# Performance work log

Measured on AMD Instinct MI355X. Metric: run time of the kernel, lower is better.

The kernel has to match this reference:

```python
import jax, jax.numpy as jnp
import numpy as np
import math

D_MODEL = 256
NUM_SLOTS = 128
RANK = 32
STEPS = 6
VOCAB = 32000
SEQ = 512
BATCH = 8
LN_EPS = 1e-5


def setup_inputs() -> dict:
    key = jax.random.key(0)
    ks = jax.random.split(key, 16)
    std = 0.02
    inp = {
        "input_ids": jax.random.randint(ks[0], (BATCH, SEQ), 0, VOCAB),
        "attention_mask": jnp.ones((BATCH, SEQ), dtype=jnp.int32),
        "token_emb": jax.random.normal(ks[1], (VOCAB, D_MODEL), jnp.float32) * std,
        "pos_emb": jax.random.normal(ks[2], (SEQ, D_MODEL), jnp.float32) * std,
        "H": jax.random.normal(ks[3], (NUM_SLOTS, D_MODEL), jnp.float32) / math.sqrt(D_MODEL),
        "W_source": jax.random.normal(ks[4], (NUM_SLOTS, NUM_SLOTS, D_MODEL, RANK), jnp.float32) * std,
        "W_target": jax.random.normal(ks[5], (NUM_SLOTS, NUM_SLOTS, RANK, D_MODEL), jnp.float32) * std,
        "Wq_in": jax.random.normal(ks[6], (D_MODEL, D_MODEL), jnp.float32) / math.sqrt(D_MODEL),
        "Wk_slots": jax.random.normal(ks[7], (D_MODEL, D_MODEL), jnp.float32) / math.sqrt(D_MODEL),
        "Wv_in": jax.random.normal(ks[8], (D_MODEL, D_MODEL), jnp.float32) / math.sqrt(D_MODEL),
        "Wq_out": jax.random.normal(ks[9], (D_MODEL, D_MODEL), jnp.float32) / math.sqrt(D_MODEL),
        "Wk_fin": jax.random.normal(ks[10], (D_MODEL, D_MODEL), jnp.float32) / math.sqrt(D_MODEL),
        "Wv_fin": jax.random.normal(ks[11], (D_MODEL, D_MODEL), jnp.float32) / math.sqrt(D_MODEL),
        "W_out_proj": jax.random.normal(ks[12], (VOCAB, D_MODEL), jnp.float32) / math.sqrt(D_MODEL),
        "ln_scale": jnp.ones((STEPS, D_MODEL), jnp.float32),
        "ln_bias": jnp.zeros((STEPS, D_MODEL), jnp.float32),
    }
    return inp


def _layernorm(x, g, b):
    mu = jnp.mean(x, axis=-1, keepdims=True)
    var = jnp.var(x, axis=-1, keepdims=True)
    return (x - mu) / jnp.sqrt(var + LN_EPS) * g + b


def _forward(input_ids, attention_mask, token_emb, pos_emb, H, W_source, W_target,
             Wq_in, Wk_slots, Wv_in, Wq_out, Wk_fin, Wv_fin, W_out_proj, ln_scale, ln_bias):
    B, L = input_ids.shape
    scale = 1.0 / math.sqrt(D_MODEL)
    # embeddings (dropout is identity in eval)
    X = token_emb[input_ids] + pos_emb[jnp.arange(L)][None]  # (B,L,D)
    # compress: input tokens -> slots
    Q_in = X @ Wq_in.T                      # (B,L,D)
    K_sl = H @ Wk_slots.T                   # (S,D)
    V_in = X @ Wv_in.T                      # (B,L,D)
    A = jax.nn.softmax(Q_in @ K_sl.T * scale, axis=-1)  # (B,L,S)
    m = attention_mask.astype(A.dtype)[..., None]
    A = A * m
    A = A / (jnp.sum(A, axis=1, keepdims=True) + 1e-8)
    IR = jnp.einsum('bls,bld->bsd', A, V_in)            # (B,S,D)
    H_state = H[None] + IR                               # (B,S,D)

    off_diag = (1.0 - jnp.eye(NUM_SLOTS, dtype=H_state.dtype))  # (S,S)

    def step(h, lnp):
        g, b = lnp
        # bilinear slot-to-slot influence; contract directly, no (B,S,S,D) expand of h
        inter = jnp.einsum('bid,ijdr->bijr', h, W_source)        # (B,S,S,R)
        out = jnp.einsum('bijr,ijrd->bijd', inter, W_target)     # (B,S,S,D)
        infl = jnp.einsum('bijd,ij->bjd', out, off_diag)         # mask diag + sum over i
        h = _layernorm(h + jax.nn.relu(infl), g, b)
        return h, None

    H_state, _ = jax.lax.scan(step, H_state, (ln_scale, ln_bias))

    # expand: slots -> tokens
    Q_out = X @ Wq_out.T                   # (B,L,D)
    K_f = H_state @ Wk_fin.T               # (B,S,D)
    V_f = H_state @ Wv_fin.T               # (B,S,D)
    A2 = jax.nn.softmax(jnp.einsum('bld,bsd->bls', Q_out, K_f) * scale, axis=-1)
    Y = jnp.einsum('bls,bsd->bld', A2, V_f)
    logits = Y @ W_out_proj.T              # (B,L,V)
    return logits


def reference(input_ids, attention_mask, token_emb, pos_emb, H, W_source, W_target,
              Wq_in, Wk_slots, Wv_in, Wq_out, Wk_fin, Wv_fin, W_out_proj, ln_scale, ln_bias):
    return _forward(input_ids, attention_mask, token_emb, pos_emb, H, W_source, W_target,
                    Wq_in, Wk_slots, Wv_in, Wq_out, Wk_fin, Wv_fin, W_out_proj, ln_scale, ln_bias)
```

## Files before the change

kernel.cpp:

```cpp
#include <hip/hip_runtime.h>
#include <hip/hip_bf16.h>
#include <math.h>

#define D_MODEL 256
#define NUM_SLOTS 128
#define RANK 32
#define N_STEPS 6
#define VOCAB 32000
#define SEQ 512
#define BATCH 8
#define NTOK (BATCH*SEQ)
#define LN_EPS 1e-5f
#define SM_SCALE 0.0625f
#define IGROUPS 8
#define IPG (NUM_SLOTS/IGROUPS)

typedef __attribute__((ext_vector_type(8))) short bf16x8;
typedef __attribute__((ext_vector_type(8))) _Float16 f16x8;
typedef __attribute__((ext_vector_type(4))) float f32x4;

#define GLD_LDS16(g, l) __builtin_amdgcn_global_load_lds( \
    (const __attribute__((address_space(1))) unsigned int*)(g), \
    (__attribute__((address_space(3))) unsigned int*)(l), 16, 0, 0)

__device__ inline unsigned short f2bf(float x) {
    unsigned u = __float_as_uint(x);
    unsigned r = u + 0x7fff + ((u >> 16) & 1);
    return (unsigned short)(r >> 16);
}
__device__ inline float bf2f(unsigned short h) {
    return __uint_as_float(((unsigned)h) << 16);
}
__device__ inline unsigned pk2(float a, float b) {
    auto v = __builtin_amdgcn_cvt_pkrtz(a, b);
    union { decltype(v) x; unsigned u; } c;
    c.x = v;
    return c.u;
}
__device__ inline unsigned short f2h(float x) {
    union { _Float16 h; unsigned short u; } c;
    c.h = (_Float16)x;
    return c.u;
}
__device__ inline float h2f(unsigned short u) {
    union { unsigned short u; _Float16 h; } c;
    c.u = u;
    return (float)c.h;
}

__global__ __launch_bounds__(256) void k_embed(const int* __restrict__ ids,
        const float* __restrict__ tok, const float* __restrict__ pos,
        float* __restrict__ X) {
    int bl = blockIdx.x;
    int d  = threadIdx.x;
    int l  = bl % SEQ;
    int id = ids[bl];
    X[(size_t)bl*D_MODEL + d] = tok[(size_t)id*D_MODEL + d] + pos[l*D_MODEL + d];
}

__global__ __launch_bounds__(256) void k_gemm_nt(const float* __restrict__ A,
        const float* __restrict__ B, float* __restrict__ C, int M, int N, int K) {
    __shared__ float As[32][64];
    __shared__ float Bs[32][64];
    int bm = blockIdx.x * 64, bn = blockIdx.y * 64;
    int t = threadIdx.x;
    int tm = (t & 15) * 4, tn = (t >> 4) * 4;
    float acc[4][4] = {};
    for (int k0 = 0; k0 < K; k0 += 32) {
        #pragma unroll
        for (int r = 0; r < 8; ++r) {
            int idx = r*256 + t;
            int m = idx >> 5, k = idx & 31;
            As[k][m] = A[(size_t)(bm+m)*K + k0 + k];
        }
        #pragma unroll
        for (int r = 0; r < 8; ++r) {
            int idx = r*256 + t;
            int n = idx >> 5, k = idx & 31;
            Bs[k][n] = B[(size_t)(bn+n)*K + k0 + k];
        }
        __syncthreads();
        #pragma unroll
        for (int k = 0; k < 32; ++k) {
            float4 a4 = *(const float4*)&As[k][tm];
            float4 b4 = *(const float4*)&Bs[k][tn];
            float a[4] = {a4.x,a4.y,a4.z,a4.w};
            float b[4] = {b4.x,b4.y,b4.z,b4.w};
            #pragma unroll
            for (int i = 0; i < 4; ++i)
                #pragma unroll
                for (int jj = 0; jj < 4; ++jj)
                    acc[i][jj] += a[i]*b[jj];
        }
        __syncthreads();
    }
    #pragma unroll
    for (int i = 0; i < 4; ++i) {
        float4 v = make_float4(acc[i][0],acc[i][1],acc[i][2],acc[i][3]);
        *(float4*)&C[(size_t)(bm+tm+i)*N + bn+tn] = v;
    }
}

__global__ __launch_bounds__(256) void k_gemm3(const float* __restrict__ A,
        const float* __restrict__ B0, const float* __restrict__ B1,
        const float* __restrict__ B2, float* __restrict__ C0,
        float* __restrict__ C1, float* __restrict__ C2) {
    const int K = D_MODEL, N = D_MODEL;
    const float* B = blockIdx.z == 0 ? B0 : (blockIdx.z == 1 ? B1 : B2);
    float* C = blockIdx.z == 0 ? C0 : (blockIdx.z == 1 ? C1 : C2);
    __shared__ float As[32][64];
    __shared__ float Bs[32][64];
    int bm = blockIdx.x * 64, bn = blockIdx.y * 64;
    int t = threadIdx.x;
    int tm = (t & 15) * 4, tn = (t >> 4) * 4;
    float acc[4][4] = {};
    for (int k0 = 0; k0 < K; k0 += 32) {
        #pragma unroll
        for (int r = 0; r < 8; ++r) {
            int idx = r*256 + t;
            int m = idx >> 5, k = idx & 31;
            As[k][m] = A[(size_t)(bm+m)*K + k0 + k];
        }
        #pragma unroll
        for (int r = 0; r < 8; ++r) {
            int idx = r*256 + t;
            int n = idx >> 5, k = idx & 31;
            Bs[k][n] = B[(size_t)(bn+n)*K + k0 + k];
        }
        __syncthreads();
        #pragma unroll
        for (int k = 0; k < 32; ++k) {
            float4 a4 = *(const float4*)&As[k][tm];
            float4 b4 = *(const float4*)&Bs[k][tn];
            float a[4] = {a4.x,a4.y,a4.z,a4.w};
            float b[4] = {b4.x,b4.y,b4.z,b4.w};
            #pragma unroll
            for (int i = 0; i < 4; ++i)
                #pragma unroll
                for (int jj = 0; jj < 4; ++jj)
                    acc[i][jj] += a[i]*b[jj];
        }
        __syncthreads();
    }
    #pragma unroll
    for (int i = 0; i < 4; ++i) {
        float4 v = make_float4(acc[i][0],acc[i][1],acc[i][2],acc[i][3]);
        *(float4*)&C[(size_t)(bm+tm+i)*N + bn+tn] = v;
    }
}

__global__ __launch_bounds__(256) void k_kfvf(const float* __restrict__ A,
        const float* __restrict__ B0, const float* __restrict__ B1,
        float* __restrict__ C0, float* __restrict__ C1) {
    const int K = D_MODEL, N = D_MODEL;
    const float* B = blockIdx.z == 0 ? B0 : B1;
    float* C = blockIdx.z == 0 ? C0 : C1;
    __shared__ float As[32][64];
    __shared__ float Bs[32][64];
    int bm = blockIdx.x * 64, bn = blockIdx.y * 64;
    int t = threadIdx.x;
    int tm = (t & 15) * 4, tn = (t >> 4) * 4;
    float acc[4][4] = {};
    for (int k0 = 0; k0 < K; k0 += 32) {
        #pragma unroll
        for (int r = 0; r < 8; ++r) {
            int idx = r*256 + t;
            int m = idx >> 5, k = idx & 31;
            As[k][m] = A[(size_t)(bm+m)*K + k0 + k];
        }
        #pragma unroll
        for (int r = 0; r < 8; ++r) {
            int idx = r*256 + t;
            int n = idx >> 5, k = idx & 31;
            Bs[k][n] = B[(size_t)(bn+n)*K + k0 + k];
        }
        __syncthreads();
        #pragma unroll
        for (int k = 0; k < 32; ++k) {
            float4 a4 = *(const float4*)&As[k][tm];
            float4 b4 = *(const float4*)&Bs[k][tn];
            float a[4] = {a4.x,a4.y,a4.z,a4.w};
            float b[4] = {b4.x,b4.y,b4.z,b4.w};
            #pragma unroll
            for (int i = 0; i < 4; ++i)
                #pragma unroll
                for (int jj = 0; jj < 4; ++jj)
                    acc[i][jj] += a[i]*b[jj];
        }
        __syncthreads();
    }
    #pragma unroll
    for (int i = 0; i < 4; ++i) {
        float4 v = make_float4(acc[i][0],acc[i][1],acc[i][2],acc[i][3]);
        *(float4*)&C[(size_t)(bm+tm+i)*N + bn+tn] = v;
    }
}

__global__ __launch_bounds__(256) void k_split16(const float* __restrict__ in,
        unsigned short* __restrict__ o, int n4) {
    int i = blockIdx.x*256 + threadIdx.x;
    if (i >= n4) return;
    float4 v = ((const float4*)in)[i];
    ushort4 h;
    h.x = f2h(v.x); h.y = f2h(v.y); h.z = f2h(v.z); h.w = f2h(v.w);
    ((ushort4*)o)[i] = h;
}

__global__ __launch_bounds__(256) void k_logits(
        const unsigned short* __restrict__ Ahg,
        const unsigned short* __restrict__ Bhg, float* __restrict__ C) {
    __shared__ unsigned short lds[2*8192];
    int bm = blockIdx.x * 128, bn = blockIdx.y * 128;
    int t = threadIdx.x;
    int w = t >> 6, l = t & 63;
    int wr = w >> 1, wc = w & 1;
    int lr = l & 15, lk = l >> 4;
    f32x4 acc[4][4];
    #pragma unroll
    for (int mi = 0; mi < 4; ++mi)
        #pragma unroll
        for (int ni = 0; ni < 4; ++ni)
            acc[mi][ni] = (f32x4){0.f,0.f,0.f,0.f};

    for (int kc = 0; kc < 4; ++kc) {
        if (kc) __syncthreads();
        #pragma unroll
        for (int i = 0; i < 4; ++i) {
            int c = t + i*256;
            int row = c >> 3, c8 = c & 7;
            size_t ga = (size_t)(bm+row)*256 + kc*64 + c8*8;
            size_t gb = (size_t)(bn+row)*256 + kc*64 + c8*8;
            GLD_LDS16(Ahg + ga, &lds[c*8]);
            GLD_LDS16(Bhg + gb, &lds[8192 + c*8]);
        }
        __syncthreads();
        #pragma unroll
        for (int s = 0; s < 2; ++s) {
            f16x8 ah[4], bh[4];
            #pragma unroll
            for (int mi = 0; mi < 4; ++mi) {
                int off = (wr*64 + mi*16 + lr)*64 + s*32 + lk*8;
                ah[mi] = *(const f16x8*)&lds[off];
            }
            #pragma unroll
            for (int ni = 0; ni < 4; ++ni) {
                int off = (wc*64 + ni*16 + lr)*64 + s*32 + lk*8;
                bh[ni] = *(const f16x8*)&lds[8192 + off];
            }
            #pragma unroll
            for (int mi = 0; mi < 4; ++mi)
                #pragma unroll
                for (int ni = 0; ni < 4; ++ni)
                    acc[mi][ni] = __builtin_amdgcn_mfma_f32_16x16x32_f16(ah[mi], bh[ni], acc[mi][ni], 0, 0, 0);
        }
    }
    #pragma unroll
    for (int mi = 0; mi < 4; ++mi)
        #pragma unroll
        for (int ni = 0; ni < 4; ++ni) {
            int col = bn + wc*64 + ni*16 + lr;
            #pragma unroll
            for (int r = 0; r < 4; ++r) {
                int row = bm + wr*64 + mi*16 + lk*4 + r;
                C[(size_t)row*VOCAB + col] = acc[mi][ni][r];
            }
        }
}

__global__ __launch_bounds__(128) void k_softmax_mask(float* __restrict__ A,
        const int* __restrict__ mask) {
    int row = blockIdx.x;
    int s = threadIdx.x;
    __shared__ float red[128];
    float v = A[(size_t)row*NUM_SLOTS + s] * SM_SCALE;
    red[s] = v; __syncthreads();
    for (int o = 64; o > 0; o >>= 1) { if (s < o) red[s] = fmaxf(red[s], red[s+o]); __syncthreads(); }
    float mx = red[0]; __syncthreads();
    float e = expf(v - mx);
    red[s] = e; __syncthreads();
    for (int o = 64; o > 0; o >>= 1) { if (s < o) red[s] += red[s+o]; __syncthreads(); }
    float sum = red[0];
    float m = (float)mask[row];
    A[(size_t)row*NUM_SLOTS + s] = e / sum * m;
}

__global__ __launch_bounds__(128) void k_colsum(const float* __restrict__ A,
        float* __restrict__ csp) {
    int b = blockIdx.x; int ch = blockIdx.y; int s = threadIdx.x;
    const float* Ab = A + ((size_t)b*SEQ + ch*64)*NUM_SLOTS + s;
    float a0 = 0.f, a1 = 0.f, a2 = 0.f, a3 = 0.f;
    #pragma unroll
    for (int l = 0; l < 64; l += 4) {
        a0 += Ab[(size_t)(l+0)*NUM_SLOTS];
        a1 += Ab[(size_t)(l+1)*NUM_SLOTS];
        a2 += Ab[(size_t)(l+2)*NUM_SLOTS];
        a3 += Ab[(size_t)(l+3)*NUM_SLOTS];
    }
    csp[(b*8 + ch)*NUM_SLOTS + s] = (a0+a1) + (a2+a3);
}

__global__ __launch_bounds__(256) void k_ir(const float* __restrict__ A,
        const float* __restrict__ V, const float* __restrict__ H,
        const float* __restrict__ csp, float* __restrict__ Hs,
        unsigned short* __restrict__ Hs16) {
    int bs = blockIdx.x; int b = bs >> 7; int s = bs & 127;
    int d = threadIdx.x;
    float sum = 1e-8f;
    #pragma unroll
    for (int p = 0; p < 8; ++p) sum += csp[(b*8 + p)*NUM_SLOTS + s];
    float inv = 1.0f / sum;
    const float* Ab = A + (size_t)b*SEQ*NUM_SLOTS + s;
    const float* Vb = V + (size_t)b*SEQ*D_MODEL + d;
    float a0 = 0.f, a1 = 0.f, a2 = 0.f, a3 = 0.f;
    for (int l = 0; l < SEQ; l += 4) {
        a0 += Ab[(size_t)(l+0)*NUM_SLOTS] * Vb[(size_t)(l+0)*D_MODEL];
        a1 += Ab[(size_t)(l+1)*NUM_SLOTS] * Vb[(size_t)(l+1)*D_MODEL];
        a2 += Ab[(size_t)(l+2)*NUM_SLOTS] * Vb[(size_t)(l+2)*D_MODEL];
        a3 += Ab[(size_t)(l+3)*NUM_SLOTS] * Vb[(size_t)(l+3)*D_MODEL];
    }
    float acc = (a0+a1) + (a2+a3);
    float v = H[s*D_MODEL + d] + acc * inv;
    Hs[(size_t)bs*D_MODEL + d] = v;
    Hs16[(size_t)bs*D_MODEL + d] = f2h(v);
}

__global__ __launch_bounds__(256) void k_convert(const float* __restrict__ Ws,
        const float* __restrict__ Wt, unsigned short* __restrict__ WF) {
    int i = blockIdx.x, j = blockIdx.y, z = blockIdx.z;
    int t = threadIdx.x, w = t >> 6, l = t & 63;
    __shared__ float lds[4*1056];
    float* lw = &lds[w*1056];
    size_t sBase = ((size_t)i*128 + j)*8192;
    size_t pOut = ((size_t)j*128 + i)*16384;
    int g = l >> 4, c = l & 15;
    if (z < 2) {
        int ks = z*4 + w;
        const float4* s4 = (const float4*)(Ws + sBase) + ks*256;
        #pragma unroll
        for (int q = 0; q < 4; ++q) {
            int idx = q*64 + l;
            float4 v = s4[idx];
            *(float4*)&lw[(idx>>3)*33 + 4*(idx&7)] = v;
        }
        asm volatile("s_waitcnt lgkmcnt(0)" ::: "memory");
        bool diag = (i == j);
        #pragma unroll
        for (int mt = 0; mt < 2; ++mt) {
            union { f16x8 v; } o;
            #pragma unroll
            for (int e = 0; e < 8; ++e) {
                float f = diag ? 0.f : lw[(g*8 + e)*33 + mt*16 + c];
                o.v[e] = (_Float16)f;
            }
            *(f16x8*)(WF + pOut + (size_t)((ks*2 + mt)*64 + l)*8) = o.v;
        }
    } else {
        int p0 = (z - 2)*8 + w*2;
        const float4* s4 = (const float4*)(Wt + sBase);
        #pragma unroll
        for (int q = 0; q < 4; ++q) {
            int idx = q*64 + l;
            int r = idx >> 3, c8 = idx & 7;
            float4 v = s4[r*64 + p0*4 + c8];
            *(float4*)&lw[r*33 + 4*c8] = v;
        }
        asm volatile("s_waitcnt lgkmcnt(0)" ::: "memory");
        #pragma unroll
        for (int dn = 0; dn < 2; ++dn) {
            int nt = p0 + dn;
            union { f16x8 v; } o;
            #pragma unroll
            for (int e = 0; e < 8; ++e)
                o.v[e] = (_Float16)lw[(g*8 + e)*33 + dn*16 + c];
            *(f16x8*)(WF + pOut + 8192 + (size_t)(nt*64 + l)*8) = o.v;
        }
    }
}

__global__ __launch_bounds__(256, 4) void k_pairs_mfma(const unsigned short* __restrict__ h16,
        const unsigned short* __restrict__ WF, float* __restrict__ part) {
    __shared__ unsigned short lds[2*10240];
    int j = blockIdx.x, g = blockIdx.y;
    int t = threadIdx.x, w = t >> 6, l = t & 63;
    int lg = l >> 4, c = l & 15;
    const unsigned short* pbase = WF + ((size_t)j*128 + g*16)*16384;

    {
        const unsigned short* src = pbase;
        #pragma unroll
        for (int q = 0; q < 4; ++q)
            GLD_LDS16(src + (size_t)(q*256 + t)*8, &lds[(q*256 + t)*8]);
        const unsigned short* hsrc = h16 + ((size_t)(t&7)*NUM_SLOTS + g*16)*D_MODEL + (t>>3)*8;
        GLD_LDS16(hsrc, &lds[8192 + t*8]);
    }
    __builtin_amdgcn_sched_barrier(0);
    f16x8 bqn[4];
    #pragma unroll
    for (int nt = 0; nt < 4; ++nt)
        bqn[nt] = *(const f16x8*)(pbase + 8192 + (size_t)((w*4+nt)*64 + l)*8);
    __builtin_amdgcn_sched_barrier(0);

    f32x4 acc[4];
    #pragma unroll
    for (int nt = 0; nt < 4; ++nt) acc[nt] = (f32x4){0.f,0.f,0.f,0.f};
    f16x8 hzero;
    #pragma unroll
    for (int e = 0; e < 8; ++e) hzero[e] = (_Float16)0.f;

    #pragma unroll 2
    for (int ii = 0; ii < 16; ++ii) {
        int cur = ii & 1;
        asm volatile("s_waitcnt vmcnt(4) lgkmcnt(0)" ::: "memory");
        __builtin_amdgcn_s_barrier();
        __builtin_amdgcn_sched_barrier(0);
        if (ii < 15) {
            const unsigned short* src = pbase + (size_t)(ii+1)*16384;
            unsigned short* dst = &lds[(cur^1)*10240];
            #pragma unroll
            for (int q = 0; q < 4; ++q)
                GLD_LDS16(src + (size_t)(q*256 + t)*8, dst + (size_t)(q*256 + t)*8);
            const unsigned short* hsrc = h16 + ((size_t)(t&7)*NUM_SLOTS + (g*16+ii+1))*D_MODEL + (t>>3)*8;
            GLD_LDS16(hsrc, dst + 8192 + (size_t)t*8);
        }
        __builtin_amdgcn_sched_barrier(0);
        f16x8 bq[4];
        #pragma unroll
        for (int nt = 0; nt < 4; ++nt) bq[nt] = bqn[nt];
        if (ii < 15) {
            const unsigned short* bp = pbase + (size_t)(ii+1)*16384 + 8192;
            #pragma unroll
            for (int nt = 0; nt < 4; ++nt)
                bqn[nt] = *(const f16x8*)(bp + (size_t)((w*4+nt)*64 + l)*8);
        }
        const unsigned short* buf = &lds[cur*10240];
        f32x4 d1[2];
        d1[0] = (f32x4){0.f,0.f,0.f,0.f};
        d1[1] = (f32x4){0.f,0.f,0.f,0.f};
        #pragma unroll
        for (int ks = 0; ks < 8; ++ks) {
            f16x8 a0 = *(const f16x8*)(buf + (size_t)((ks*2+0)*64 + l)*8);
            f16x8 a1 = *(const f16x8*)(buf + (size_t)((ks*2+1)*64 + l)*8);
            f16x8 hv = *(const f16x8*)(buf + 8192 + (size_t)(((ks*4+lg)*8 + (c&7)))*8);
            f16x8 hb = (c < 8) ? hv : hzero;
            d1[0] = __builtin_amdgcn_mfma_f32_16x16x32_f16(a0, hb, d1[0], 0, 0, 0);
            d1[1] = __builtin_amdgcn_mfma_f32_16x16x32_f16(a1, hb, d1[1], 0, 0, 0);
        }
        unsigned q0 = pk2(d1[0][0], d1[0][1]);
        unsigned q1 = pk2(d1[0][2], d1[0][3]);
        unsigned s0 = pk2(d1[1][0], d1[1][1]);
        unsigned s1 = pk2(d1[1][2], d1[1][3]);
        int srcLo = 32*(lg & 1) + c;
        int srcHi = srcLo + 16;
        unsigned a0s = (unsigned)__shfl((int)q0, srcLo, 64);
        unsigned a1s = (unsigned)__shfl((int)q1, srcLo, 64);
        unsigned a2s = (unsigned)__shfl((int)q0, srcHi, 64);
        unsigned a3s = (unsigned)__shfl((int)q1, srcHi, 64);
        unsigned b0s = (unsigned)__shfl((int)s0, srcLo, 64);
        unsigned b1s = (unsigned)__shfl((int)s1, srcLo, 64);
        unsigned b2s = (unsigned)__shfl((int)s0, srcHi, 64);
        unsigned b3s = (unsigned)__shfl((int)s1, srcHi, 64);
        bool himt = ((lg >> 1) & 1);
        union { unsigned u[4]; f16x8 v; } A2u;
        A2u.u[0] = himt ? b0s : a0s;
        A2u.u[1] = himt ? b1s : a1s;
        A2u.u[2] = himt ? b2s : a2s;
        A2u.u[3] = himt ? b3s : a3s;
        #pragma unroll
        for (int nt = 0; nt < 4; ++nt)
            acc[nt] = __builtin_amdgcn_mfma_f32_16x16x32_f16(A2u.v, bq[nt], acc[nt], 0, 0, 0);
    }
    if (lg < 2) {
        #pragma unroll
        for (int nt = 0; nt < 4; ++nt) {
            int d = (w*4 + nt)*16 + c;
            #pragma unroll
            for (int r = 0; r < 4; ++r) {
                int b = lg*4 + r;
                part[(((size_t)g*BATCH + b)*NUM_SLOTS + j)*D_MODEL + d] = acc[nt][r];
            }
        }
    }
}

__global__ __launch_bounds__(256) void k_pairs(const float* __restrict__ h,
        const float* __restrict__ Ws, const float* __restrict__ Wt,
        float* __restrict__ part) {
    int j = blockIdx.x;
    int g = blockIdx.y;
    int t = threadIdx.x;
    __shared__ float sh_h[BATCH][D_MODEL];
    __shared__ float sh_inter[BATCH][RANK];
    float acc[BATCH];
    #pragma unroll
    for (int b = 0; b < BATCH; ++b) acc[b] = 0.f;
    int tb = t >> 5, tr = t & 31;
    for (int ii = 0; ii < IPG; ++ii) {
        int i = g*IPG + ii;
        if (i == j) continue;
        #pragma unroll
        for (int b = 0; b < BATCH; ++b)
            sh_h[b][t] = h[((size_t)b*NUM_SLOTS + i)*D_MODEL + t];
        __syncthreads();
        const float* ws = Ws + ((size_t)i*NUM_SLOTS + j)*(D_MODEL*RANK);
        float accA = 0.f;
        #pragma unroll 8
        for (int d = 0; d < D_MODEL; ++d)
            accA += sh_h[tb][d] * ws[(size_t)d*RANK + tr];
        sh_inter[tb][tr] = accA;
        __syncthreads();
        const float* wt = Wt + ((size_t)i*NUM_SLOTS + j)*(RANK*D_MODEL);
        #pragma unroll 8
        for (int r = 0; r < RANK; ++r) {
            float w = wt[(size_t)r*D_MODEL + t];
            #pragma unroll
            for (int b = 0; b < BATCH; ++b) acc[b] += sh_inter[b][r] * w;
        }
        __syncthreads();
    }
    #pragma unroll
    for (int b = 0; b < BATCH; ++b)
        part[(((size_t)g*BATCH + b)*NUM_SLOTS + j)*D_MODEL + t] = acc[b];
}

__global__ __launch_bounds__(256) void k_ln(float* __restrict__ h,
        unsigned short* __restrict__ h16, const float* __restrict__ part,
        const float* __restrict__ gma, const float* __restrict__ bta) {
    int bj = blockIdx.x;
    int t = threadIdx.x;
    int b = bj >> 7, j = bj & 127;
    __shared__ float red[256];
    float v = 0.f;
    #pragma unroll
    for (int g = 0; g < IGROUPS; ++g)
        v += part[(((size_t)g*BATCH + b)*NUM_SLOTS + j)*D_MODEL + t];
    float x = h[(size_t)bj*D_MODEL + t] + fmaxf(v, 0.f);
    red[t] = x; __syncthreads();
    for (int o = 128; o > 0; o >>= 1) { if (t < o) red[t] += red[t+o]; __syncthreads(); }
    float mu = red[0] * (1.0f/D_MODEL); __syncthreads();
    float dx = x - mu;
    red[t] = dx*dx; __syncthreads();
    for (int o = 128; o > 0; o >>= 1) { if (t < o) red[t] += red[t+o]; __syncthreads(); }
    float var = red[0] * (1.0f/D_MODEL);
    float outv = dx * rsqrtf(var + LN_EPS) * gma[t] + bta[t];
    h[(size_t)bj*D_MODEL + t] = outv;
    h16[(size_t)bj*D_MODEL + t] = f2h(outv);
}

__global__ __launch_bounds__(256) void k_attn2y(const float* __restrict__ Q,
        const float* __restrict__ Kf, const float* __restrict__ Vf,
        unsigned short* __restrict__ Yh) {
    int bl = blockIdx.x; int b = bl / SEQ;
    int t = threadIdx.x;
    __shared__ float q[D_MODEL];
    __shared__ float prt[2][128];
    __shared__ float a[128];
    __shared__ float red[128];
    q[t] = Q[(size_t)bl*D_MODEL + t];
    __syncthreads();
    int s = t & 127, hf = t >> 7;
    const float* kf = Kf + ((size_t)b*NUM_SLOTS + s)*D_MODEL + hf*128;
    float accp = 0.f;
    #pragma unroll 8
    for (int d = 0; d < 128; ++d) accp += q[hf*128 + d]*kf[d];
    prt[hf][s] = accp;
    __syncthreads();
    float v = 0.f;
    if (t < 128) { v = (prt[0][t] + prt[1][t]) * SM_SCALE; red[t] = v; }
    __syncthreads();
    for (int o = 64; o > 0; o >>= 1) { if (t < o) red[t] = fmaxf(red[t], red[t+o]); __syncthreads(); }
    float mx = red[0]; __syncthreads();
    if (t < 128) { float e = expf(v - mx); a[t] = e; red[t] = e; }
    __syncthreads();
    for (int o = 64; o > 0; o >>= 1) { if (t < o) red[t] += red[t+o]; __syncthreads(); }
    float inv = 1.0f / red[0];
    __syncthreads();
    const float* vf = Vf + (size_t)b*NUM_SLOTS*D_MODEL + t;
    float y0 = 0.f, y1 = 0.f, y2 = 0.f, y3 = 0.f;
    #pragma unroll
    for (int s2 = 0; s2 < NUM_SLOTS; s2 += 4) {
        y0 += a[s2+0]*vf[(size_t)(s2+0)*D_MODEL];
        y1 += a[s2+1]*vf[(size_t)(s2+1)*D_MODEL];
        y2 += a[s2+2]*vf[(size_t)(s2+2)*D_MODEL];
        y3 += a[s2+3]*vf[(size_t)(s2+3)*D_MODEL];
    }
    float y = ((y0+y1) + (y2+y3)) * inv;
    Yh[(size_t)bl*D_MODEL + t] = f2h(y);
}

extern "C" void kernel_launch(void* const* d_in, const int* in_sizes, int n_in,
                              void* d_out, int out_size, void* d_ws, size_t ws_size,
                              hipStream_t stream) {
    const int*   ids    = (const int*)d_in[0];
    const int*   amask  = (const int*)d_in[1];
    const float* tok    = (const float*)d_in[2];
    const float* pos    = (const float*)d_in[3];
    const float* Hin    = (const float*)d_in[4];
    const float* Ws     = (const float*)d_in[5];
    const float* Wt     = (const float*)d_in[6];
    const float* Wq_in  = (const float*)d_in[7];
    const float* Wk_sl  = (const float*)d_in[8];
    const float* Wv_in  = (const float*)d_in[9];
    const float* Wq_out = (const float*)d_in[10];
    const float* Wk_fin = (const float*)d_in[11];
    const float* Wv_fin = (const float*)d_in[12];
    const float* Wop    = (const float*)d_in[13];
    const float* lnsc   = (const float*)d_in[14];
    const float* lnbs   = (const float*)d_in[15];
    float* out = (float*)d_out;

    const size_t WF_USH = (size_t)16384 * 16384;
    const size_t F32_FLOATS = 18600000ULL;
    const bool useF16 = ws_size >= WF_USH*2 + F32_FLOATS*4 + 256;

    unsigned short* WF = (unsigned short*)d_ws;
    float* ws = useF16 ? (float*)(WF + WF_USH) : (float*)d_ws;

    float* X    = ws;
    float* Qin  = X    + (size_t)NTOK*D_MODEL;
    float* Vin  = Qin  + (size_t)NTOK*D_MODEL;
    float* Ksl  = Vin  + (size_t)NTOK*D_MODEL;
    float* Asc  = Ksl  + (size_t)NUM_SLOTS*D_MODEL;
    float* csp  = Asc  + (size_t)NTOK*NUM_SLOTS;
    float* Hst  = csp  + (size_t)BATCH*8*NUM_SLOTS;
    float* part = Hst  + (size_t)BATCH*NUM_SLOTS*D_MODEL;
    float* Qout = part + (size_t)IGROUPS*BATCH*NUM_SLOTS*D_MODEL;
    float* Kf   = Qout + (size_t)NTOK*D_MODEL;
    float* Vf   = Kf   + (size_t)BATCH*NUM_SLOTS*D_MODEL;
    float* A2   = Vf   + (size_t)BATCH*NUM_SLOTS*D_MODEL;
    float* Yb   = A2   + (size_t)NTOK*NUM_SLOTS;
    unsigned short* Yh = (unsigned short*)(Yb + (size_t)NTOK*D_MODEL);
    unsigned short* Yl = Yh + (size_t)NTOK*D_MODEL;
    unsigned short* Wf16 = Yl + (size_t)NTOK*D_MODEL;
    unsigned short* Hst16 = Wf16 + (size_t)VOCAB*D_MODEL;

    if (useF16)
        k_convert<<<dim3(128, 128, 4), 256, 0, stream>>>(Ws, Wt, WF);
    k_split16<<<(VOCAB*D_MODEL/4 + 255)/256, 256, 0, stream>>>(Wop, Wf16, VOCAB*D_MODEL/4);

    k_embed<<<NTOK, 256, 0, stream>>>(ids, tok, pos, X);
    k_gemm3<<<dim3(NTOK/64, 4, 3), 256, 0, stream>>>(X, Wq_in, Wv_in, Wq_out, Qin, Vin, Qout);
    k_gemm_nt<<<dim3(2, 4), 256, 0, stream>>>(Hin, Wk_sl, Ksl, NUM_SLOTS, D_MODEL, D_MODEL);
    k_gemm_nt<<<dim3(NTOK/64, 2), 256, 0, stream>>>(Qin, Ksl, Asc, NTOK, NUM_SLOTS, D_MODEL);
    k_softmax_mask<<<NTOK, 128, 0, stream>>>(Asc, amask);
    k_colsum<<<dim3(BATCH, 8), 128, 0, stream>>>(Asc, csp);
    k_ir<<<BATCH*NUM_SLOTS, 256, 0, stream>>>(Asc, Vin, Hin, csp, Hst, Hst16);
    for (int st = 0; st < N_STEPS; ++st) {
        if (useF16)
            k_pairs_mfma<<<dim3(NUM_SLOTS, IGROUPS), 256, 0, stream>>>(Hst16, WF, part);
        else
            k_pairs<<<dim3(NUM_SLOTS, IGROUPS), 256, 0, stream>>>(Hst, Ws, Wt, part);
        k_ln<<<BATCH*NUM_SLOTS, 256, 0, stream>>>(Hst, Hst16, part, lnsc + st*D_MODEL, lnbs + st*D_MODEL);
    }
    k_kfvf<<<dim3(BATCH*NUM_SLOTS/64, 4, 2), 256, 0, stream>>>(Hst, Wk_fin, Wv_fin, Kf, Vf);
    k_attn2y<<<NTOK, 256, 0, stream>>>(Qout, Kf, Vf, Yh);
    k_logits<<<dim3(NTOK/128, VOCAB/128), 256, 0, stream>>>(Yh, Wf16, out);
}
```

Measured before the change: 1.426 ms.

## Fuse embedding into projection GEMM and attention scores with softmax, drop colsum

New measurement: 1.423 ms. No clear change (-0.2%).

```diff
diff --git a/kernel.cpp b/kernel.cpp
--- a/kernel.cpp
+++ b/kernel.cpp
@@ -23,14 +23,6 @@
     (const __attribute__((address_space(1))) unsigned int*)(g), \
     (__attribute__((address_space(3))) unsigned int*)(l), 16, 0, 0)
 
-__device__ inline unsigned short f2bf(float x) {
-    unsigned u = __float_as_uint(x);
-    unsigned r = u + 0x7fff + ((u >> 16) & 1);
-    return (unsigned short)(r >> 16);
-}
-__device__ inline float bf2f(unsigned short h) {
-    return __uint_as_float(((unsigned)h) << 16);
-}
 __device__ inline unsigned pk2(float a, float b) {
     auto v = __builtin_amdgcn_cvt_pkrtz(a, b);
     union { decltype(v) x; unsigned u; } c;
@@ -41,21 +33,6 @@
     union { _Float16 h; unsigned short u; } c;
     c.h = (_Float16)x;
     return c.u;
-}
-__device__ inline float h2f(unsigned short u) {
-    union { unsigned short u; _Float16 h; } c;
-    c.u = u;
-    return (float)c.h;
-}
-
-__global__ __launch_bounds__(256) void k_embed(const int* __restrict__ ids,
-        const float* __restrict__ tok, const float* __restrict__ pos,
-        float* __restrict__ X) {
-    int bl = blockIdx.x;
-    int d  = threadIdx.x;
-    int l  = bl % SEQ;
-    int id = ids[bl];
-    X[(size_t)bl*D_MODEL + d] = tok[(size_t)id*D_MODEL + d] + pos[l*D_MODEL + d];
 }
 
 __global__ __launch_bounds__(256) void k_gemm_nt(const float* __restrict__ A,
@@ -101,7 +78,8 @@
     }
 }
 
-__global__ __launch_bounds__(256) void k_gemm3(const float* __restrict__ A,
+__global__ __launch_bounds__(256) void k_gemm3e(const int* __restrict__ ids,
+        const float* __restrict__ tok, const float* __restrict__ pos,
         const float* __restrict__ B0, const float* __restrict__ B1,
         const float* __restrict__ B2, float* __restrict__ C0,
         float* __restrict__ C1, float* __restrict__ C2) {
@@ -110,8 +88,11 @@
     float* C = blockIdx.z == 0 ? C0 : (blockIdx.z == 1 ? C1 : C2);
     __shared__ float As[32][64];
     __shared__ float Bs[32][64];
+    __shared__ int sid[64];
     int bm = blockIdx.x * 64, bn = blockIdx.y * 64;
     int t = threadIdx.x;
+    if (t < 64) sid[t] = ids[bm + t];
+    __syncthreads();
     int tm = (t & 15) * 4, tn = (t >> 4) * 4;
     float acc[4][4] = {};
     for (int k0 = 0; k0 < K; k0 += 32) {
@@ -119,7 +100,8 @@
         for (int r = 0; r < 8; ++r) {
             int idx = r*256 + t;
             int m = idx >> 5, k = idx & 31;
-            As[k][m] = A[(size_t)(bm+m)*K + k0 + k];
+            int gm = bm + m;
+            As[k][m] = tok[(size_t)sid[m]*K + k0 + k] + pos[(gm & (SEQ-1))*K + k0 + k];
         }
         #pragma unroll
         for (int r = 0; r < 8; ++r) {
@@ -149,51 +131,30 @@
     }
 }
 
-__global__ __launch_bounds__(256) void k_kfvf(const float* __restrict__ A,
-        const float* __restrict__ B0, const float* __restrict__ B1,
-        float* __restrict__ C0, float* __restrict__ C1) {
-    const int K = D_MODEL, N = D_MODEL;
-    const float* B = blockIdx.z == 0 ? B0 : B1;
-    float* C = blockIdx.z == 0 ? C0 : C1;
-    __shared__ float As[32][64];
-    __shared__ float Bs[32][64];
-    int bm = blockIdx.x * 64, bn = blockIdx.y * 64;
-    int t = threadIdx.x;
-    int tm = (t & 15) * 4, tn = (t >> 4) * 4;
-    float acc[4][4] = {};
-    for (int k0 = 0; k0 < K; k0 += 32) {
-        #pragma unroll
-        for (int r = 0; r < 8; ++r) {
-            int idx = r*256 + t;
-            int m = idx >> 5, k = idx & 31;
-            As[k][m] = A[(size_t)(bm+m)*K + k0 + k];
-        }
-        #pragma unroll
-        for (int r = 0; r < 8; ++r) {
-            int idx = r*256 + t;
-            int n = idx >> 5, k = idx & 31;
-            Bs[k][n] = B[(size_t)(bn+n)*K + k0 + k];
-        }
-        __syncthreads();
-        #pragma unroll
-        for (int k = 0; k < 32; ++k) {
-            float4 a4 = *(const float4*)&As[k][tm];
-            float4 b4 = *(const float4*)&Bs[k][tn];
-            float a[4] = {a4.x,a4.y,a4.z,a4.w};
-            float b[4] = {b4.x,b4.y,b4.z,b4.w};
-            #pragma unroll
-            for (int i = 0; i < 4; ++i)
-                #pragma unroll
-                for (int jj = 0; jj < 4; ++jj)
-                    acc[i][jj] += a[i]*b[jj];
-        }
-        __syncthreads();
-    }
-    #pragma unroll
-    for (int i = 0; i < 4; ++i) {
-        float4 v = make_float4(acc[i][0],acc[i][1],acc[i][2],acc[i][3]);
-        *(float4*)&C[(size_t)(bm+tm+i)*N + bn+tn] = v;
-    }
+__global__ __launch_bounds__(128) void k_attn1(const float* __restrict__ Qin,
+        const float* __restrict__ Ksl, const int* __restrict__ mask,
+        float* __restrict__ A) {
+    int bl = blockIdx.x;
+    int s = threadIdx.x;
+    __shared__ float q[D_MODEL];
+    __shared__ float red[128];
+    q[s]       = Qin[(size_t)bl*D_MODEL + s];
+    q[s + 128] = Qin[(size_t)bl*D_MODEL + s + 128];
+    __syncthreads();
+    const float* kr = Ksl + (size_t)s*D_MODEL;
+    float acc = 0.f;
+    #pragma unroll 8
+    for (int d = 0; d < D_MODEL; ++d) acc += q[d]*kr[d];
+    acc *= SM_SCALE;
+    red[s] = acc; __syncthreads();
+    for (int o = 64; o > 0; o >>= 1) { if (s < o) red[s] = fmaxf(red[s], red[s+o]); __syncthreads(); }
+    float mx = red[0]; __syncthreads();
+    float e = expf(acc - mx);
+    red[s] = e; __syncthreads();
+    for (int o = 64; o > 0; o >>= 1) { if (s < o) red[s] += red[s+o]; __syncthreads(); }
+    float sum = red[0];
+    float m = (float)mask[bl];
+    A[(size_t)bl*NUM_SLOTS + s] = e / sum * m;
 }
 
 __global__ __launch_bounds__(256) void k_split16(const float* __restrict__ in,
@@ -267,59 +228,29 @@
         }
 }
 
-__global__ __launch_bounds__(128) void k_softmax_mask(float* __restrict__ A,
-        const int* __restrict__ mask) {
-    int row = blockIdx.x;
-    int s = threadIdx.x;
-    __shared__ float red[128];
-    float v = A[(size_t)row*NUM_SLOTS + s] * SM_SCALE;
-    red[s] = v; __syncthreads();
-    for (int o = 64; o > 0; o >>= 1) { if (s < o) red[s] = fmaxf(red[s], red[s+o]); __syncthreads(); }
-    float mx = red[0]; __syncthreads();
-    float e = expf(v - mx);
-    red[s] = e; __syncthreads();
-    for (int o = 64; o > 0; o >>= 1) { if (s < o) red[s] += red[s+o]; __syncthreads(); }
-    float sum = red[0];
-    float m = (float)mask[row];
-    A[(size_t)row*NUM_SLOTS + s] = e / sum * m;
-}
-
-__global__ __launch_bounds__(128) void k_colsum(const float* __restrict__ A,
-        float* __restrict__ csp) {
-    int b = blockIdx.x; int ch = blockIdx.y; int s = threadIdx.x;
-    const float* Ab = A + ((size_t)b*SEQ + ch*64)*NUM_SLOTS + s;
-    float a0 = 0.f, a1 = 0.f, a2 = 0.f, a3 = 0.f;
-    #pragma unroll
-    for (int l = 0; l < 64; l += 4) {
-        a0 += Ab[(size_t)(l+0)*NUM_SLOTS];
-        a1 += Ab[(size_t)(l+1)*NUM_SLOTS];
-        a2 += Ab[(size_t)(l+2)*NUM_SLOTS];
-        a3 += Ab[(size_t)(l+3)*NUM_SLOTS];
-    }
-    csp[(b*8 + ch)*NUM_SLOTS + s] = (a0+a1) + (a2+a3);
-}
-
 __global__ __launch_bounds__(256) void k_ir(const float* __restrict__ A,
         const float* __restrict__ V, const float* __restrict__ H,
-        const float* __restrict__ csp, float* __restrict__ Hs,
-        unsigned short* __restrict__ Hs16) {
+        float* __restrict__ Hs, unsigned short* __restrict__ Hs16) {
     int bs = blockIdx.x; int b = bs >> 7; int s = bs & 127;
     int d = threadIdx.x;
-    float sum = 1e-8f;
-    #pragma unroll
-    for (int p = 0; p < 8; ++p) sum += csp[(b*8 + p)*NUM_SLOTS + s];
-    float inv = 1.0f / sum;
     const float* Ab = A + (size_t)b*SEQ*NUM_SLOTS + s;
     const float* Vb = V + (size_t)b*SEQ*D_MODEL + d;
     float a0 = 0.f, a1 = 0.f, a2 = 0.f, a3 = 0.f;
+    float s0 = 0.f, s1 = 0.f, s2 = 0.f, s3 = 0.f;
     for (int l = 0; l < SEQ; l += 4) {
-        a0 += Ab[(size_t)(l+0)*NUM_SLOTS] * Vb[(size_t)(l+0)*D_MODEL];
-        a1 += Ab[(size_t)(l+1)*NUM_SLOTS] * Vb[(size_t)(l+1)*D_MODEL];
-        a2 += Ab[(size_t)(l+2)*NUM_SLOTS] * Vb[(size_t)(l+2)*D_MODEL];
-        a3 += Ab[(size_t)(l+3)*NUM_SLOTS] * Vb[(size_t)(l+3)*D_MODEL];
-    }
+        float w0 = Ab[(size_t)(l+0)*NUM_SLOTS];
+        float w1 = Ab[(size_t)(l+1)*NUM_SLOTS];
+        float w2 = Ab[(size_t)(l+2)*NUM_SLOTS];
+        float w3 = Ab[(size_t)(l+3)*NUM_SLOTS];
+        a0 += w0 * Vb[(size_t)(l+0)*D_MODEL];
+        a1 += w1 * Vb[(size_t)(l+1)*D_MODEL];
+        a2 += w2 * Vb[(size_t)(l+2)*D_MODEL];
+        a3 += w3 * Vb[(size_t)(l+3)*D_MODEL];
+        s0 += w0; s1 += w1; s2 += w2; s3 += w3;
+    }
+    float asum = (s0+s1) + (s2+s3) + 1e-8f;
     float acc = (a0+a1) + (a2+a3);
-    float v = H[s*D_MODEL + d] + acc * inv;
+    float v = H[s*D_MODEL + d] + acc / asum;
     Hs[(size_t)bs*D_MODEL + d] = v;
     Hs16[(size_t)bs*D_MODEL + d] = f2h(v);
 }
@@ -482,46 +413,6 @@
     }
 }
 
-__global__ __launch_bounds__(256) void k_pairs(const float* __restrict__ h,
-        const float* __restrict__ Ws, const float* __restrict__ Wt,
-        float* __restrict__ part) {
-    int j = blockIdx.x;
-    int g = blockIdx.y;
-    int t = threadIdx.x;
-    __shared__ float sh_h[BATCH][D_MODEL];
-    __shared__ float sh_inter[BATCH][RANK];
-    float acc[BATCH];
-    #pragma unroll
-    for (int b = 0; b < BATCH; ++b) acc[b] = 0.f;
-    int tb = t >> 5, tr = t & 31;
-    for (int ii = 0; ii < IPG; ++ii) {
-        int i = g*IPG + ii;
-        if (i == j) continue;
-        #pragma unroll
-        for (int b = 0; b < BATCH; ++b)
-            sh_h[b][t] = h[((size_t)b*NUM_SLOTS + i)*D_MODEL + t];
-        __syncthreads();
-        const float* ws = Ws + ((size_t)i*NUM_SLOTS + j)*(D_MODEL*RANK);
-        float accA = 0.f;
-        #pragma unroll 8
-        for (int d = 0; d < D_MODEL; ++d)
-            accA += sh_h[tb][d] * ws[(size_t)d*RANK + tr];
-        sh_inter[tb][tr] = accA;
-        __syncthreads();
-        const float* wt = Wt + ((size_t)i*NUM_SLOTS + j)*(RANK*D_MODEL);
-        #pragma unroll 8
-        for (int r = 0; r < RANK; ++r) {
-            float w = wt[(size_t)r*D_MODEL + t];
-            #pragma unroll
-            for (int b = 0; b < BATCH; ++b) acc[b] += sh_inter[b][r] * w;
-        }
-        __syncthreads();
-    }
-    #pragma unroll
-    for (int b = 0; b < BATCH; ++b)
-        part[(((size_t)g*BATCH + b)*NUM_SLOTS + j)*D_MODEL + t] = acc[b];
-}
-
 __global__ __launch_bounds__(256) void k_ln(float* __restrict__ h,
         unsigned short* __restrict__ h16, const float* __restrict__ part,
         const float* __restrict__ gma, const float* __restrict__ bta) {
@@ -544,6 +435,53 @@
     float outv = dx * rsqrtf(var + LN_EPS) * gma[t] + bta[t];
     h[(size_t)bj*D_MODEL + t] = outv;
     h16[(size_t)bj*D_MODEL + t] = f2h(outv);
+}
+
+__global__ __launch_bounds__(256) void k_kfvf(const float* __restrict__ A,
+        const float* __restrict__ B0, const float* __restrict__ B1,
+        float* __restrict__ C0, float* __restrict__ C1) {
+    const int K = D_MODEL, N = D_MODEL;
+    const float* B = blockIdx.z == 0 ? B0 : B1;
+    float* C = blockIdx.z == 0 ? C0 : C1;
+    __shared__ float As[32][64];
+    __shared__ float Bs[32][64];
+    int bm = blockIdx.x * 64, bn = blockIdx.y * 64;
+    int t = threadIdx.x;
+    int tm = (t & 15) * 4, tn = (t >> 4) * 4;
+    float acc[4][4] = {};
+    for (int k0 = 0; k0 < K; k0 += 32) {
+        #pragma unroll
+        for (int r = 0; r < 8; ++r) {
+            int idx = r*256 + t;
+            int m = idx >> 5, k = idx & 31;
+            As[k][m] = A[(size_t)(bm+m)*K + k0 + k];
+        }
+        #pragma unroll
+        for (int r = 0; r < 8; ++r) {
+            int idx = r*256 + t;
+            int n = idx >> 5, k = idx & 31;
+            Bs[k][n] = B[(size_t)(bn+n)*K + k0 + k];
+        }
+        __syncthreads();
+        #pragma unroll
+        for (int k = 0; k < 32; ++k) {
+            float4 a4 = *(const float4*)&As[k][tm];
+            float4 b4 = *(const float4*)&Bs[k][tn];
+            float a[4] = {a4.x,a4.y,a4.z,a4.w};
+            float b[4] = {b4.x,b4.y,b4.z,b4.w};
+            #pragma unroll
+            for (int i = 0; i < 4; ++i)
+                #pragma unroll
+                for (int jj = 0; jj < 4; ++jj)
+                    acc[i][jj] += a[i]*b[jj];
+        }
+        __syncthreads();
+    }
+    #pragma unroll
+    for (int i = 0; i < 4; ++i) {
+        float4 v = make_float4(acc[i][0],acc[i][1],acc[i][2],acc[i][3]);
+        *(float4*)&C[(size_t)(bm+tm+i)*N + bn+tn] = v;
+    }
 }
 
 __global__ __launch_bounds__(256) void k_attn2y(const float* __restrict__ Q,
@@ -609,11 +547,8 @@
     float* out = (float*)d_out;
 
     const size_t WF_USH = (size_t)16384 * 16384;
-    const size_t F32_FLOATS = 18600000ULL;
-    const bool useF16 = ws_size >= WF_USH*2 + F32_FLOATS*4 + 256;
-
     unsigned short* WF = (unsigned short*)d_ws;
-    float* ws = useF16 ? (float*)(WF + WF_USH) : (float*)d_ws;
+    float* ws = (float*)(WF + WF_USH);
 
     float* X    = ws;
     float* Qin  = X    + (size_t)NTOK*D_MODEL;
@@ -633,22 +568,16 @@
     unsigned short* Wf16 = Yl + (size_t)NTOK*D_MODEL;
     unsigned short* Hst16 = Wf16 + (size_t)VOCAB*D_MODEL;
 
-    if (useF16)
-        k_convert<<<dim3(128, 128, 4), 256, 0, stream>>>(Ws, Wt, WF);
+    k_convert<<<dim3(128, 128, 4), 256, 0, stream>>>(Ws, Wt, WF);
     k_split16<<<(VOCAB*D_MODEL/4 + 255)/256, 256, 0, stream>>>(Wop, Wf16, VOCAB*D_MODEL/4);
 
-    k_embed<<<NTOK, 256, 0, stream>>>(ids, tok, pos, X);
-    k_gemm3<<<dim3(NTOK/64, 4, 3), 256, 0, stream>>>(X, Wq_in, Wv_in, Wq_out, Qin, Vin, Qout);
+    k_gemm3e<<<dim3(NTOK/64, 4, 3), 256, 0, stream>>>(ids, tok, pos,
+            Wq_in, Wv_in, Wq_out, Qin, Vin, Qout);
     k_gemm_nt<<<dim3(2, 4), 256, 0, stream>>>(Hin, Wk_sl, Ksl, NUM_SLOTS, D_MODEL, D_MODEL);
-    k_gemm_nt<<<dim3(NTOK/64, 2), 256, 0, stream>>>(Qin, Ksl, Asc, NTOK, NUM_SLOTS, D_MODEL);
-    k_softmax_mask<<<NTOK, 128, 0, stream>>>(Asc, amask);
-    k_colsum<<<dim3(BATCH, 8), 128, 0, stream>>>(Asc, csp);
-    k_ir<<<BATCH*NUM_SLOTS, 256, 0, stream>>>(Asc, Vin, Hin, csp, Hst, Hst16);
+    k_attn1<<<NTOK, 128, 0, stream>>>(Qin, Ksl, amask, Asc);
+    k_ir<<<BATCH*NUM_SLOTS, 256, 0, stream>>>(Asc, Vin, Hin, Hst, Hst16);
     for (int st = 0; st < N_STEPS; ++st) {
-        if (useF16)
-            k_pairs_mfma<<<dim3(NUM_SLOTS, IGROUPS), 256, 0, stream>>>(Hst16, WF, part);
-        else
-            k_pairs<<<dim3(NUM_SLOTS, IGROUPS), 256, 0, stream>>>(Hst, Ws, Wt, part);
+        k_pairs_mfma<<<dim3(NUM_SLOTS, IGROUPS), 256, 0, stream>>>(Hst16, WF, part);
         k_ln<<<BATCH*NUM_SLOTS, 256, 0, stream>>>(Hst, Hst16, part, lnsc + st*D_MODEL, lnbs + st*D_MODEL);
     }
     k_kfvf<<<dim3(BATCH*NUM_SLOTS/64, 4, 2), 256, 0, stream>>>(Hst, Wk_fin, Wv_fin, Kf, Vf);
```
